# Performance work log

Hardware: AMD Instinct MI355X
Metric: run time of the kernel (lower is better)

The kernel has to match this reference:

```python
import jax, jax.numpy as jnp
import numpy as np


def setup_inputs() -> dict:
    key = jax.random.key(0)
    kq, kk, kv, kb = jax.random.split(key, 4)
    B, H, S, D = 4, 16, 1024, 64
    return {
        "query": jax.random.normal(kq, (B, H, S, D), dtype=jnp.float32),
        "key": jax.random.normal(kk, (B, H, S, D), dtype=jnp.float32),
        "value": jax.random.normal(kv, (B, H, S, D), dtype=jnp.float32),
        "bias_mask": jax.random.normal(kb, (1, 1, S, S), dtype=jnp.float32),
    }


def reference(query, key, value, bias_mask):
    d_k = query.shape[-1]
    scale = 1.0 / jnp.sqrt(jnp.asarray(d_k, dtype=query.dtype))
    # scores: [B, H, Sq, Sk]
    scores = jnp.einsum("bhqd,bhkd->bhqk", query, key) * scale
    scores = scores + bias_mask
    attn_weights = jax.nn.softmax(scores, axis=-1)
    output = jnp.einsum("bhqk,bhkd->bhqd", attn_weights, value)
    return (output, attn_weights)
```

## Files before the change

kernel.cpp:

```cpp
#include <hip/hip_runtime.h>

constexpr int SEQ = 1024;
constexpr int DH  = 64;
constexpr int QR  = 32;
constexpr int KT  = 128;
constexpr int NKT = SEQ / KT;

constexpr int SK0 = 0;
constexpr int SK1 = 16384;
constexpr int SV0 = 32768;
constexpr int SV1 = 49152;
constexpr int SPO = 65536;
constexpr int SQO = 73728;
constexpr int SRL = 77824;
constexpr int SMEM_BYTES = 78080;

typedef __bf16 bf16x8 __attribute__((ext_vector_type(8)));
typedef __bf16 bf16x4 __attribute__((ext_vector_type(4)));
typedef float  f32x4  __attribute__((ext_vector_type(4)));

__device__ __forceinline__ char* kadr(char* s, int base, int row, int colB) {
    return s + base + row * 128 + (colB ^ ((row & 7) << 4));
}
__device__ __forceinline__ char* vadr(char* s, int base, int row, int colB) {
    return s + base + row * 256 + (colB ^ ((row & 15) << 4));
}

__global__ __launch_bounds__(256, 2)
void attn_flash_kernel(const float* __restrict__ Q, const float* __restrict__ K,
                       const float* __restrict__ V, const float* __restrict__ bias,
                       float* __restrict__ out, float* __restrict__ attn)
{
    __shared__ __align__(16) char smem[SMEM_BYTES];

    const int tid = threadIdx.x;
    const int l   = tid & 63;
    const int w   = tid >> 6;
    const int qt  = w & 1;
    const int ch  = w >> 1;
    const int lm  = l & 15;
    const int lq  = l >> 4;
    const int j4  = lm & 3;
    const int m0v = lm & 12;
    const int head = blockIdx.x & 63;
    const int q0   = (blockIdx.x >> 6) * QR;
    const float scale = 0.125f;

    const float* Qh = Q + (size_t)head * SEQ * DH;
    const float* Kh = K + (size_t)head * SEQ * DH;
    const float* Vh = V + (size_t)head * SEQ * DH;
    float* outh  = out  + (size_t)head * SEQ * DH;
    float* attnh = attn + (size_t)head * SEQ * SEQ;

    const int srow = tid >> 4;
    const int sdg  = tid & 15;
    const int vkb  = tid & 31;
    const int vdb0 = tid >> 5;

    f32x4 kv[8], vv[2][4];
    #pragma unroll
    for (int i = 0; i < 8; ++i)
        kv[i] = *(const f32x4*)(Kh + (size_t)(srow + 16 * i) * DH + sdg * 4);
    #pragma unroll
    for (int i = 0; i < 2; ++i)
        #pragma unroll
        for (int jj = 0; jj < 4; ++jj)
            vv[i][jj] = *(const f32x4*)(Vh + (size_t)(vkb * 4 + jj) * DH + (vdb0 + 8 * i) * 4);

    #pragma unroll
    for (int i = 0; i < 2; ++i) {
        int row = srow + 16 * i;
        f32x4 v = *(const f32x4*)(Qh + (size_t)(q0 + row) * DH + sdg * 4);
        bf16x4 b;
        b[0] = (__bf16)v[0]; b[1] = (__bf16)v[1]; b[2] = (__bf16)v[2]; b[3] = (__bf16)v[3];
        *(bf16x4*)kadr(smem, SQO, row, sdg * 8) = b;
    }
    #pragma unroll
    for (int i = 0; i < 8; ++i) {
        bf16x4 b;
        b[0] = (__bf16)kv[i][0]; b[1] = (__bf16)kv[i][1];
        b[2] = (__bf16)kv[i][2]; b[3] = (__bf16)kv[i][3];
        *(bf16x4*)kadr(smem, SK0, srow + 16 * i, sdg * 8) = b;
    }
    #pragma unroll
    for (int i = 0; i < 2; ++i) {
        int d0 = (vdb0 + 8 * i) * 4;
        #pragma unroll
        for (int jj = 0; jj < 4; ++jj) {
            bf16x4 b;
            b[0] = (__bf16)vv[i][0][jj]; b[1] = (__bf16)vv[i][1][jj];
            b[2] = (__bf16)vv[i][2][jj]; b[3] = (__bf16)vv[i][3][jj];
            *(bf16x4*)vadr(smem, SV0, d0 + jj, vkb * 8) = b;
        }
    }
    __syncthreads();

    bf16x8 aQ0 = *(const bf16x8*)kadr(smem, SQO, qt * 16 + lm, lq * 16);
    bf16x8 aQ1 = *(const bf16x8*)kadr(smem, SQO, qt * 16 + lm, 64 + lq * 16);

    f32x4 xs[NKT][4];
    float ssum[4] = {0.f, 0.f, 0.f, 0.f};
    f32x4 oacc[2] = {{0,0,0,0},{0,0,0,0}};
    const int dtb    = ch * 2;
    const int rowg_l = qt * 16 + lq * 4;

    #pragma unroll
    for (int kt = 0; kt < NKT; ++kt) {
        const int curK = (kt & 1) ? SK1 : SK0;
        const int curV = (kt & 1) ? SV1 : SV0;
        const int nxtK = (kt & 1) ? SK0 : SK1;
        const int nxtV = (kt & 1) ? SV0 : SV1;

        if (kt < NKT - 1) {
            #pragma unroll
            for (int i = 0; i < 8; ++i)
                kv[i] = *(const f32x4*)(Kh + (size_t)((kt + 1) * KT + srow + 16 * i) * DH + sdg * 4);
            #pragma unroll
            for (int i = 0; i < 2; ++i)
                #pragma unroll
                for (int jj = 0; jj < 4; ++jj)
                    vv[i][jj] = *(const f32x4*)(Vh + (size_t)((kt + 1) * KT + vkb * 4 + jj) * DH + (vdb0 + 8 * i) * 4);
        }
        const int colg = kt * KT + ch * 64 + lm;
        float bb[4][4];
        #pragma unroll
        for (int r = 0; r < 4; ++r) {
            const float* brow = bias + (size_t)(q0 + rowg_l + r) * SEQ + colg;
            bb[r][0] = brow[0]; bb[r][1] = brow[16]; bb[r][2] = brow[32]; bb[r][3] = brow[48];
        }

        f32x4 acc[4] = {{0,0,0,0},{0,0,0,0},{0,0,0,0},{0,0,0,0}};
        __builtin_amdgcn_s_setprio(1);
        #pragma unroll
        for (int c = 0; c < 4; ++c) {
            bf16x8 bf = *(const bf16x8*)kadr(smem, curK, (ch * 4 + c) * 16 + lm, lq * 16);
            acc[c] = __builtin_amdgcn_mfma_f32_16x16x32_bf16(aQ0, bf, acc[c], 0, 0, 0);
        }
        #pragma unroll
        for (int c = 0; c < 4; ++c) {
            bf16x8 bf = *(const bf16x8*)kadr(smem, curK, (ch * 4 + c) * 16 + lm, 64 + lq * 16);
            acc[c] = __builtin_amdgcn_mfma_f32_16x16x32_bf16(aQ1, bf, acc[c], 0, 0, 0);
        }
        __builtin_amdgcn_s_setprio(0);

        #pragma unroll
        for (int r = 0; r < 4; ++r) {
            float e0 = __expf(acc[0][r] * scale + bb[r][0]);
            float e1 = __expf(acc[1][r] * scale + bb[r][1]);
            float e2 = __expf(acc[2][r] * scale + bb[r][2]);
            float e3 = __expf(acc[3][r] * scale + bb[r][3]);
            ssum[r] += (e0 + e1) + (e2 + e3);
            xs[kt][0][r] = e0; xs[kt][1][r] = e1; xs[kt][2][r] = e2; xs[kt][3][r] = e3;
        }

        __syncthreads();

        if (kt < NKT - 1) {
            #pragma unroll
            for (int i = 0; i < 8; ++i) {
                bf16x4 b;
                b[0] = (__bf16)kv[i][0]; b[1] = (__bf16)kv[i][1];
                b[2] = (__bf16)kv[i][2]; b[3] = (__bf16)kv[i][3];
                *(bf16x4*)kadr(smem, nxtK, srow + 16 * i, sdg * 8) = b;
            }
            #pragma unroll
            for (int i = 0; i < 2; ++i) {
                int d0 = (vdb0 + 8 * i) * 4;
                #pragma unroll
                for (int jj = 0; jj < 4; ++jj) {
                    bf16x4 b;
                    b[0] = (__bf16)vv[i][0][jj]; b[1] = (__bf16)vv[i][1][jj];
                    b[2] = (__bf16)vv[i][2][jj]; b[3] = (__bf16)vv[i][3][jj];
                    *(bf16x4*)vadr(smem, nxtV, d0 + jj, vkb * 8) = b;
                }
            }
        }
        #pragma unroll
        for (int r = 0; r < 4; ++r) {
            #pragma unroll
            for (int c = 0; c < 4; ++c)
                *(__bf16*)vadr(smem, SPO, rowg_l + r, ch * 128 + 32 * c + 2 * lm) =
                    (__bf16)xs[kt][c][r];
        }
        __syncthreads();

        __builtin_amdgcn_s_setprio(1);
        #pragma unroll
        for (int ks = 0; ks < 4; ++ks) {
            bf16x8 af = *(const bf16x8*)vadr(smem, SPO, qt * 16 + lm, ks * 64 + lq * 16);
            #pragma unroll
            for (int c = 0; c < 2; ++c) {
                bf16x8 bf = *(const bf16x8*)vadr(smem, curV, (dtb + c) * 16 + lm, ks * 64 + lq * 16);
                oacc[c] = __builtin_amdgcn_mfma_f32_16x16x32_bf16(af, bf, oacc[c], 0, 0, 0);
            }
        }
        __builtin_amdgcn_s_setprio(0);
    }

    #pragma unroll
    for (int r = 0; r < 4; ++r) {
        float s = ssum[r];
        #pragma unroll
        for (int off = 1; off < 16; off <<= 1)
            s += __shfl_xor(s, off);
        ssum[r] = s;
    }
    float* sRLp = (float*)(smem + SRL);
    if (lm == 0) {
        #pragma unroll
        for (int r = 0; r < 4; ++r)
            sRLp[ch * 32 + rowg_l + r] = ssum[r];
    }
    __syncthreads();
    float linv[4];
    #pragma unroll
    for (int r = 0; r < 4; ++r)
        linv[r] = 1.0f / (sRLp[rowg_l + r] + sRLp[32 + rowg_l + r]);

    const bool b0 = (lm & 1) != 0;
    const bool b1 = (lm & 2) != 0;
    const int  rowt = qt * 16 + lq * 4 + j4;
    #pragma unroll
    for (int kt = 0; kt < NKT; ++kt) {
        #pragma unroll
        for (int c = 0; c < 4; ++c) {
            float v0 = xs[kt][c][0] * linv[0];
            float v1 = xs[kt][c][1] * linv[1];
            float v2 = xs[kt][c][2] * linv[2];
            float v3 = xs[kt][c][3] * linv[3];
            { float a = b0 ? v0 : v1; float t = __shfl_xor(a, 1); if (b0) v0 = t; else v1 = t; }
            { float a = b0 ? v2 : v3; float t = __shfl_xor(a, 1); if (b0) v2 = t; else v3 = t; }
            { float a = b1 ? v0 : v2; float t = __shfl_xor(a, 2); if (b1) v0 = t; else v2 = t; }
            { float a = b1 ? v1 : v3; float t = __shfl_xor(a, 2); if (b1) v1 = t; else v3 = t; }
            f32x4 wv; wv[0] = v0; wv[1] = v1; wv[2] = v2; wv[3] = v3;
            float* ap = attnh + (size_t)(q0 + rowt) * SEQ + kt * KT + ch * 64 + 16 * c + m0v;
            __builtin_nontemporal_store(wv, (f32x4*)ap);
        }
    }

    #pragma unroll
    for (int c = 0; c < 2; ++c)
        #pragma unroll
        for (int r = 0; r < 4; ++r)
            __builtin_nontemporal_store(oacc[c][r] * linv[r],
                outh + (size_t)(q0 + rowg_l + r) * DH + (dtb + c) * 16 + lm);
}

extern "C" void kernel_launch(void* const* d_in, const int* in_sizes, int n_in,
                              void* d_out, int out_size, void* d_ws, size_t ws_size,
                              hipStream_t stream) {
    const float* Q    = (const float*)d_in[0];
    const float* K    = (const float*)d_in[1];
    const float* V    = (const float*)d_in[2];
    const float* bias = (const float*)d_in[3];
    float* out  = (float*)d_out;
    float* attn = (float*)d_out + 4 * 16 * 1024 * 64;
    dim3 grid(64 * (SEQ / QR));
    dim3 block(256);
    attn_flash_kernel<<<grid, block, 0, stream>>>(Q, K, V, bias, out, attn);
}
```

Baseline: 450.6 us.

## Split attention into QK-softmax pass and PV pass with bf16 score storage

Restructures the kernel into two phases. The first streams K tiles of 64 and keeps the exponentiated scores in registers as bf16. The second streams V and writes the normalized attention weights through a shared-memory staging buffer as coalesced row-wise stores while doing the PV MFMAs. Shared memory drops from about 78KB to 32KB and launch bounds raise occupancy to 4 blocks. Q is now loaded straight from global memory into MFMA fragments. Storing scores as bf16 lowers the precision of the returned attention weights, which may affect tolerance.

```diff
diff --git a/kernel.cpp b/kernel.cpp
--- a/kernel.cpp
+++ b/kernel.cpp
@@ -3,30 +3,27 @@
 constexpr int SEQ = 1024;
 constexpr int DH  = 64;
 constexpr int QR  = 32;
-constexpr int KT  = 128;
+constexpr int KT  = 64;
 constexpr int NKT = SEQ / KT;
 
 constexpr int SK0 = 0;
-constexpr int SK1 = 16384;
-constexpr int SV0 = 32768;
-constexpr int SV1 = 49152;
-constexpr int SPO = 65536;
-constexpr int SQO = 73728;
-constexpr int SRL = 77824;
-constexpr int SMEM_BYTES = 78080;
+constexpr int SK1 = 8192;
+constexpr int SP0 = 0;
+constexpr int SP1 = 4096;
+constexpr int SRL = 8192;
+constexpr int SV0 = 16384;
+constexpr int SV1 = 24576;
+constexpr int SMEM_BYTES = 32768;
 
 typedef __bf16 bf16x8 __attribute__((ext_vector_type(8)));
 typedef __bf16 bf16x4 __attribute__((ext_vector_type(4)));
 typedef float  f32x4  __attribute__((ext_vector_type(4)));
 
-__device__ __forceinline__ char* kadr(char* s, int base, int row, int colB) {
+__device__ __forceinline__ char* ldsa(char* s, int base, int row, int colB) {
     return s + base + row * 128 + (colB ^ ((row & 7) << 4));
 }
-__device__ __forceinline__ char* vadr(char* s, int base, int row, int colB) {
-    return s + base + row * 256 + (colB ^ ((row & 15) << 4));
-}
-
-__global__ __launch_bounds__(256, 2)
+
+__global__ __launch_bounds__(256, 4)
 void attn_flash_kernel(const float* __restrict__ Q, const float* __restrict__ K,
                        const float* __restrict__ V, const float* __restrict__ bias,
                        float* __restrict__ out, float* __restrict__ attn)
@@ -40,8 +37,6 @@
     const int ch  = w >> 1;
     const int lm  = l & 15;
     const int lq  = l >> 4;
-    const int j4  = lm & 3;
-    const int m0v = lm & 12;
     const int head = blockIdx.x & 63;
     const int q0   = (blockIdx.x >> 6) * QR;
     const float scale = 0.125f;
@@ -54,148 +49,84 @@
 
     const int srow = tid >> 4;
     const int sdg  = tid & 15;
-    const int vkb  = tid & 31;
-    const int vdb0 = tid >> 5;
-
-    f32x4 kv[8], vv[2][4];
-    #pragma unroll
-    for (int i = 0; i < 8; ++i)
+    const int vkb  = tid >> 4;
+    const int vdb  = tid & 15;
+    const int rowg_l = qt * 16 + lq * 4;
+
+    f32x4 kv[4];
+    #pragma unroll
+    for (int i = 0; i < 4; ++i)
         kv[i] = *(const f32x4*)(Kh + (size_t)(srow + 16 * i) * DH + sdg * 4);
-    #pragma unroll
-    for (int i = 0; i < 2; ++i)
-        #pragma unroll
-        for (int jj = 0; jj < 4; ++jj)
-            vv[i][jj] = *(const f32x4*)(Vh + (size_t)(vkb * 4 + jj) * DH + (vdb0 + 8 * i) * 4);
-
-    #pragma unroll
-    for (int i = 0; i < 2; ++i) {
-        int row = srow + 16 * i;
-        f32x4 v = *(const f32x4*)(Qh + (size_t)(q0 + row) * DH + sdg * 4);
-        bf16x4 b;
-        b[0] = (__bf16)v[0]; b[1] = (__bf16)v[1]; b[2] = (__bf16)v[2]; b[3] = (__bf16)v[3];
-        *(bf16x4*)kadr(smem, SQO, row, sdg * 8) = b;
-    }
-    #pragma unroll
-    for (int i = 0; i < 8; ++i) {
-        bf16x4 b;
-        b[0] = (__bf16)kv[i][0]; b[1] = (__bf16)kv[i][1];
-        b[2] = (__bf16)kv[i][2]; b[3] = (__bf16)kv[i][3];
-        *(bf16x4*)kadr(smem, SK0, srow + 16 * i, sdg * 8) = b;
-    }
-    #pragma unroll
-    for (int i = 0; i < 2; ++i) {
-        int d0 = (vdb0 + 8 * i) * 4;
-        #pragma unroll
-        for (int jj = 0; jj < 4; ++jj) {
+
+    bf16x8 aQ[2];
+    {
+        const float* qrow = Qh + (size_t)(q0 + qt * 16 + lm) * DH;
+        #pragma unroll
+        for (int ks = 0; ks < 2; ++ks) {
+            f32x4 a = *(const f32x4*)(qrow + ks * 32 + lq * 8);
+            f32x4 b = *(const f32x4*)(qrow + ks * 32 + lq * 8 + 4);
+            bf16x8 f;
+            f[0] = (__bf16)a[0]; f[1] = (__bf16)a[1]; f[2] = (__bf16)a[2]; f[3] = (__bf16)a[3];
+            f[4] = (__bf16)b[0]; f[5] = (__bf16)b[1]; f[6] = (__bf16)b[2]; f[7] = (__bf16)b[3];
+            aQ[ks] = f;
+        }
+    }
+
+    bf16x4 xsb[NKT][2];
+    float ssum[4] = {0.f, 0.f, 0.f, 0.f};
+
+    #pragma unroll
+    for (int kt = 0; kt < NKT; ++kt) {
+        const int bufK = (kt & 1) ? SK1 : SK0;
+        #pragma unroll
+        for (int i = 0; i < 4; ++i) {
             bf16x4 b;
-            b[0] = (__bf16)vv[i][0][jj]; b[1] = (__bf16)vv[i][1][jj];
-            b[2] = (__bf16)vv[i][2][jj]; b[3] = (__bf16)vv[i][3][jj];
-            *(bf16x4*)vadr(smem, SV0, d0 + jj, vkb * 8) = b;
-        }
-    }
-    __syncthreads();
-
-    bf16x8 aQ0 = *(const bf16x8*)kadr(smem, SQO, qt * 16 + lm, lq * 16);
-    bf16x8 aQ1 = *(const bf16x8*)kadr(smem, SQO, qt * 16 + lm, 64 + lq * 16);
-
-    f32x4 xs[NKT][4];
-    float ssum[4] = {0.f, 0.f, 0.f, 0.f};
-    f32x4 oacc[2] = {{0,0,0,0},{0,0,0,0}};
-    const int dtb    = ch * 2;
-    const int rowg_l = qt * 16 + lq * 4;
-
-    #pragma unroll
-    for (int kt = 0; kt < NKT; ++kt) {
-        const int curK = (kt & 1) ? SK1 : SK0;
-        const int curV = (kt & 1) ? SV1 : SV0;
-        const int nxtK = (kt & 1) ? SK0 : SK1;
-        const int nxtV = (kt & 1) ? SV0 : SV1;
+            b[0] = (__bf16)kv[i][0]; b[1] = (__bf16)kv[i][1];
+            b[2] = (__bf16)kv[i][2]; b[3] = (__bf16)kv[i][3];
+            *(bf16x4*)ldsa(smem, bufK, srow + 16 * i, sdg * 8) = b;
+        }
+        __syncthreads();
 
         if (kt < NKT - 1) {
             #pragma unroll
-            for (int i = 0; i < 8; ++i)
+            for (int i = 0; i < 4; ++i)
                 kv[i] = *(const f32x4*)(Kh + (size_t)((kt + 1) * KT + srow + 16 * i) * DH + sdg * 4);
-            #pragma unroll
-            for (int i = 0; i < 2; ++i)
-                #pragma unroll
-                for (int jj = 0; jj < 4; ++jj)
-                    vv[i][jj] = *(const f32x4*)(Vh + (size_t)((kt + 1) * KT + vkb * 4 + jj) * DH + (vdb0 + 8 * i) * 4);
-        }
-        const int colg = kt * KT + ch * 64 + lm;
-        float bb[4][4];
+        }
+        const int colg = kt * KT + ch * 32 + lm;
+        float bb[4][2];
         #pragma unroll
         for (int r = 0; r < 4; ++r) {
             const float* brow = bias + (size_t)(q0 + rowg_l + r) * SEQ + colg;
-            bb[r][0] = brow[0]; bb[r][1] = brow[16]; bb[r][2] = brow[32]; bb[r][3] = brow[48];
-        }
-
-        f32x4 acc[4] = {{0,0,0,0},{0,0,0,0},{0,0,0,0},{0,0,0,0}};
+            bb[r][0] = brow[0]; bb[r][1] = brow[16];
+        }
+
+        f32x4 acc[2] = {{0,0,0,0},{0,0,0,0}};
         __builtin_amdgcn_s_setprio(1);
         #pragma unroll
-        for (int c = 0; c < 4; ++c) {
-            bf16x8 bf = *(const bf16x8*)kadr(smem, curK, (ch * 4 + c) * 16 + lm, lq * 16);
-            acc[c] = __builtin_amdgcn_mfma_f32_16x16x32_bf16(aQ0, bf, acc[c], 0, 0, 0);
-        }
-        #pragma unroll
-        for (int c = 0; c < 4; ++c) {
-            bf16x8 bf = *(const bf16x8*)kadr(smem, curK, (ch * 4 + c) * 16 + lm, 64 + lq * 16);
-            acc[c] = __builtin_amdgcn_mfma_f32_16x16x32_bf16(aQ1, bf, acc[c], 0, 0, 0);
+        for (int ks = 0; ks < 2; ++ks) {
+            #pragma unroll
+            for (int c = 0; c < 2; ++c) {
+                bf16x8 bf = *(const bf16x8*)ldsa(smem, bufK, (ch * 2 + c) * 16 + lm, ks * 64 + lq * 16);
+                acc[c] = __builtin_amdgcn_mfma_f32_16x16x32_bf16(aQ[ks], bf, acc[c], 0, 0, 0);
+            }
         }
         __builtin_amdgcn_s_setprio(0);
 
         #pragma unroll
-        for (int r = 0; r < 4; ++r) {
-            float e0 = __expf(acc[0][r] * scale + bb[r][0]);
-            float e1 = __expf(acc[1][r] * scale + bb[r][1]);
-            float e2 = __expf(acc[2][r] * scale + bb[r][2]);
-            float e3 = __expf(acc[3][r] * scale + bb[r][3]);
-            ssum[r] += (e0 + e1) + (e2 + e3);
-            xs[kt][0][r] = e0; xs[kt][1][r] = e1; xs[kt][2][r] = e2; xs[kt][3][r] = e3;
-        }
-
-        __syncthreads();
-
-        if (kt < NKT - 1) {
-            #pragma unroll
-            for (int i = 0; i < 8; ++i) {
-                bf16x4 b;
-                b[0] = (__bf16)kv[i][0]; b[1] = (__bf16)kv[i][1];
-                b[2] = (__bf16)kv[i][2]; b[3] = (__bf16)kv[i][3];
-                *(bf16x4*)kadr(smem, nxtK, srow + 16 * i, sdg * 8) = b;
+        for (int c = 0; c < 2; ++c) {
+            #pragma unroll
+            for (int r = 0; r < 4; ++r) {
+                float e = __expf(acc[c][r] * scale + bb[r][c]);
+                ssum[r] += e;
+                xsb[kt][c][r] = (__bf16)e;
             }
-            #pragma unroll
-            for (int i = 0; i < 2; ++i) {
-                int d0 = (vdb0 + 8 * i) * 4;
-                #pragma unroll
-                for (int jj = 0; jj < 4; ++jj) {
-                    bf16x4 b;
-                    b[0] = (__bf16)vv[i][0][jj]; b[1] = (__bf16)vv[i][1][jj];
-                    b[2] = (__bf16)vv[i][2][jj]; b[3] = (__bf16)vv[i][3][jj];
-                    *(bf16x4*)vadr(smem, nxtV, d0 + jj, vkb * 8) = b;
-                }
-            }
-        }
-        #pragma unroll
-        for (int r = 0; r < 4; ++r) {
-            #pragma unroll
-            for (int c = 0; c < 4; ++c)
-                *(__bf16*)vadr(smem, SPO, rowg_l + r, ch * 128 + 32 * c + 2 * lm) =
-                    (__bf16)xs[kt][c][r];
-        }
-        __syncthreads();
-
-        __builtin_amdgcn_s_setprio(1);
-        #pragma unroll
-        for (int ks = 0; ks < 4; ++ks) {
-            bf16x8 af = *(const bf16x8*)vadr(smem, SPO, qt * 16 + lm, ks * 64 + lq * 16);
-            #pragma unroll
-            for (int c = 0; c < 2; ++c) {
-                bf16x8 bf = *(const bf16x8*)vadr(smem, curV, (dtb + c) * 16 + lm, ks * 64 + lq * 16);
-                oacc[c] = __builtin_amdgcn_mfma_f32_16x16x32_bf16(af, bf, oacc[c], 0, 0, 0);
-            }
-        }
-        __builtin_amdgcn_s_setprio(0);
-    }
+        }
+    }
+
+    f32x4 vv[4];
+    #pragma unroll
+    for (int j = 0; j < 4; ++j)
+        vv[j] = *(const f32x4*)(Vh + (size_t)(vkb * 4 + j) * DH + vdb * 4);
 
     #pragma unroll
     for (int r = 0; r < 4; ++r) {
@@ -205,6 +136,7 @@
             s += __shfl_xor(s, off);
         ssum[r] = s;
     }
+    __syncthreads();
     float* sRLp = (float*)(smem + SRL);
     if (lm == 0) {
         #pragma unroll
@@ -216,26 +148,60 @@
     #pragma unroll
     for (int r = 0; r < 4; ++r)
         linv[r] = 1.0f / (sRLp[rowg_l + r] + sRLp[32 + rowg_l + r]);
-
-    const bool b0 = (lm & 1) != 0;
-    const bool b1 = (lm & 2) != 0;
-    const int  rowt = qt * 16 + lq * 4 + j4;
+    const int arow = tid >> 3;
+    const int achk = tid & 7;
+    const float linv_s = 1.0f / (sRLp[arow] + sRLp[32 + arow]);
+
+    const int dtb = ch * 2;
+    f32x4 oacc[2] = {{0,0,0,0},{0,0,0,0}};
+
     #pragma unroll
     for (int kt = 0; kt < NKT; ++kt) {
-        #pragma unroll
-        for (int c = 0; c < 4; ++c) {
-            float v0 = xs[kt][c][0] * linv[0];
-            float v1 = xs[kt][c][1] * linv[1];
-            float v2 = xs[kt][c][2] * linv[2];
-            float v3 = xs[kt][c][3] * linv[3];
-            { float a = b0 ? v0 : v1; float t = __shfl_xor(a, 1); if (b0) v0 = t; else v1 = t; }
-            { float a = b0 ? v2 : v3; float t = __shfl_xor(a, 1); if (b0) v2 = t; else v3 = t; }
-            { float a = b1 ? v0 : v2; float t = __shfl_xor(a, 2); if (b1) v0 = t; else v2 = t; }
-            { float a = b1 ? v1 : v3; float t = __shfl_xor(a, 2); if (b1) v1 = t; else v3 = t; }
-            f32x4 wv; wv[0] = v0; wv[1] = v1; wv[2] = v2; wv[3] = v3;
-            float* ap = attnh + (size_t)(q0 + rowt) * SEQ + kt * KT + ch * 64 + 16 * c + m0v;
-            __builtin_nontemporal_store(wv, (f32x4*)ap);
-        }
+        const int bufP = (kt & 1) ? SP1 : SP0;
+        const int bufV = (kt & 1) ? SV1 : SV0;
+
+        #pragma unroll
+        for (int jj = 0; jj < 4; ++jj) {
+            bf16x4 b;
+            b[0] = (__bf16)vv[0][jj]; b[1] = (__bf16)vv[1][jj];
+            b[2] = (__bf16)vv[2][jj]; b[3] = (__bf16)vv[3][jj];
+            *(bf16x4*)ldsa(smem, bufV, vdb * 4 + jj, vkb * 8) = b;
+        }
+        #pragma unroll
+        for (int c = 0; c < 2; ++c)
+            #pragma unroll
+            for (int r = 0; r < 4; ++r)
+                *(__bf16*)ldsa(smem, bufP, rowg_l + r, (ch * 32 + c * 16 + lm) * 2) = xsb[kt][c][r];
+        __syncthreads();
+
+        if (kt < NKT - 1) {
+            #pragma unroll
+            for (int j = 0; j < 4; ++j)
+                vv[j] = *(const f32x4*)(Vh + (size_t)((kt + 1) * KT + vkb * 4 + j) * DH + vdb * 4);
+        }
+
+        {
+            bf16x4 pa = *(const bf16x4*)ldsa(smem, bufP, arow, achk * 8);
+            bf16x4 pb = *(const bf16x4*)ldsa(smem, bufP, arow, 64 + achk * 8);
+            f32x4 wa, wb;
+            #pragma unroll
+            for (int i = 0; i < 4; ++i) { wa[i] = (float)pa[i] * linv_s; wb[i] = (float)pb[i] * linv_s; }
+            float* ap = attnh + (size_t)(q0 + arow) * SEQ + kt * KT;
+            __builtin_nontemporal_store(wa, (f32x4*)(ap + achk * 4));
+            __builtin_nontemporal_store(wb, (f32x4*)(ap + 32 + achk * 4));
+        }
+
+        __builtin_amdgcn_s_setprio(1);
+        #pragma unroll
+        for (int ks = 0; ks < 2; ++ks) {
+            bf16x8 af = *(const bf16x8*)ldsa(smem, bufP, qt * 16 + lm, ks * 64 + lq * 16);
+            #pragma unroll
+            for (int c = 0; c < 2; ++c) {
+                bf16x8 bf = *(const bf16x8*)ldsa(smem, bufV, (dtb + c) * 16 + lm, ks * 64 + lq * 16);
+                oacc[c] = __builtin_amdgcn_mfma_f32_16x16x32_bf16(af, bf, oacc[c], 0, 0, 0);
+            }
+        }
+        __builtin_amdgcn_s_setprio(0);
     }
 
     #pragma unroll
```

After: 516.4 us. +14.6%, slower.
